# Kernel optimization log

Measured on AMD Instinct MI355X. Metric: run time of the kernel, lower is better.

The kernel has to match this reference:

```python
import jax, jax.numpy as jnp
import numpy as np

B, S, D, H = 4, 1024, 1024, 16
HD = D // H  # head_dim = 64


def setup_inputs() -> dict:
    key = jax.random.key(0)
    ks = jax.random.split(key, 12)
    scale = 1.0 / np.sqrt(D)
    inp = {
        "query": jax.random.normal(ks[0], (B, S, D), jnp.float32),
        "key": jax.random.normal(ks[1], (B, S, D), jnp.float32),
        "value": jax.random.normal(ks[2], (B, S, D), jnp.float32),
        "mask": jnp.zeros((B, S), dtype=bool),  # accepted but unused by the module
        "Wq": jax.random.normal(ks[3], (D, D), jnp.float32) * scale,
        "bq": jnp.zeros((D,), jnp.float32),
        "Wk": jax.random.normal(ks[4], (D, D), jnp.float32) * scale,
        "bk": jnp.zeros((D,), jnp.float32),
        "Wv": jax.random.normal(ks[5], (D, D), jnp.float32) * scale,
        "bv": jnp.zeros((D,), jnp.float32),
        "Wo": jax.random.normal(ks[6], (D, D), jnp.float32) * scale,
        "bo": jnp.zeros((D,), jnp.float32),
    }
    return inp


def _split_heads(x):
    # [B,S,D] -> [B,H,S,HD]
    b, s, _ = x.shape
    return x.reshape(b, s, H, HD).transpose(0, 2, 1, 3)


def reference(query, key, value, mask, Wq, bq, Wk, bk, Wv, bv, Wo, bo):
    b, s, _ = query.shape
    q = _split_heads(query @ Wq.T + bq)
    k = _split_heads(key @ Wk.T + bk)
    v = _split_heads(value @ Wv.T + bv)
    # dense scores, then hollow mask: triu(diag=1) and tril(diag=-1) are both
    # filled with -inf, leaving ONLY the diagonal unmasked
    scores = jnp.einsum("bhqd,bhkd->bhqk", q, k) / jnp.sqrt(jnp.float32(HD))
    diag = jnp.eye(s, dtype=bool)  # the only surviving positions
    scores = jnp.where(diag, scores, -jnp.inf)
    attn = jax.nn.softmax(scores, axis=-1)  # == identity one-hot rows
    out = jnp.einsum("bhqk,bhkd->bhqd", attn, v)
    out = out.transpose(0, 2, 1, 3).reshape(b, s, H * HD)
    return out @ Wo.T + bo
```

## Files before the change

### kernel.cpp

```cpp
#include <hip/hip_runtime.h>
#include <stdint.h>


typedef __attribute__((ext_vector_type(4))) float f32x4;
typedef __attribute__((ext_vector_type(8))) __bf16 bf16x8;
typedef __attribute__((ext_vector_type(4))) float float4v;
typedef __attribute__((ext_vector_type(8))) unsigned short ushort8;
typedef __attribute__((ext_vector_type(4))) unsigned short us4;

#define DEVINL __device__ __forceinline__

DEVINL unsigned short f2bf(float f) {
  union { float f; uint32_t u; } c; c.f = f;
  uint32_t r = c.u + 0x7FFFu + ((c.u >> 16) & 1u);
  return (unsigned short)(r >> 16);
}

#define GLD16(g, l) __builtin_amdgcn_global_load_lds( \
    (__attribute__((address_space(1))) void*)(g),     \
    (__attribute__((address_space(3))) void*)(l), 16, 0, 0)

__global__ __launch_bounds__(256) void prep(
    const float* __restrict__ V, const float* __restrict__ Wv,
    const float* __restrict__ Wo, const float* __restrict__ bv,
    const float* __restrict__ bo,
    unsigned short* __restrict__ Vb, unsigned short* __restrict__ Wob,
    unsigned short* __restrict__ WvT, float* __restrict__ bias2) {
  __shared__ unsigned short tile[64][65];
  const int b = blockIdx.x, t = threadIdx.x;
  if (b < 2560) {
    const float* src = (b < 2048) ? V : Wo;
    unsigned short* dst = (b < 2048) ? Vb : Wob;
    long off = ((long)(b < 2048 ? b : b - 2048) * 256 + t) * 8;
    float4v a = *(const float4v*)(src + off);
    float4v c = *(const float4v*)(src + off + 4);
    ushort8 o;
    o[0]=f2bf(a[0]); o[1]=f2bf(a[1]); o[2]=f2bf(a[2]); o[3]=f2bf(a[3]);
    o[4]=f2bf(c[0]); o[5]=f2bf(c[1]); o[6]=f2bf(c[2]); o[7]=f2bf(c[3]);
    *(ushort8*)(dst + off) = o;
  } else if (b < 2816) {
    const int tb = b - 2560;
    const int c0 = (tb & 15) * 64, j0 = (tb >> 4) * 64;
    const int tr = t >> 4, tc = (t & 15) * 4;
    #pragma unroll
    for (int rr = 0; rr < 4; ++rr) {
      int row = tr + rr * 16;
      float4v v = *(const float4v*)(Wv + (long)(j0 + row) * 1024 + c0 + tc);
      tile[row][tc+0] = f2bf(v[0]);
      tile[row][tc+1] = f2bf(v[1]);
      tile[row][tc+2] = f2bf(v[2]);
      tile[row][tc+3] = f2bf(v[3]);
    }
    __syncthreads();
    #pragma unroll
    for (int rr = 0; rr < 4; ++rr) {
      int crow = tr + rr * 16;
      us4 o;
      #pragma unroll
      for (int i = 0; i < 4; ++i) o[i] = tile[tc + i][crow];
      *(us4*)(WvT + (long)(c0 + crow) * 1024 + j0 + tc) = o;
    }
  } else {
    const int tb = b - 2816;
    const int w = t >> 6, lane = t & 63;
    const int row = tb * 4 + w;
    float s = 0.f;
    #pragma unroll
    for (int c = 0; c < 4; ++c) {
      int col = c * 256 + lane * 4;
      float4v a = *(const float4v*)(Wo + (long)row * 1024 + col);
      float4v x = *(const float4v*)(bv + col);
      s += a[0]*x[0] + a[1]*x[1] + a[2]*x[2] + a[3]*x[3];
    }
    #pragma unroll
    for (int off = 32; off; off >>= 1) s += __shfl_down(s, off);
    if (lane == 0) bias2[row] = s + bo[row];
  }
}

template<int BM, int BN, int NT, int WM, int WN, int OUT_BF16, int ADD_BIAS>
__global__ __launch_bounds__(NT) void gemm_nt(
    const unsigned short* __restrict__ A,
    const unsigned short* __restrict__ B,
    const float* __restrict__ bias,
    void* __restrict__ Cv) {
  constexpr int K = 1024, N = 1024;
  constexpr int NBN = N / BN;
  constexpr int SM = BM / WM, SN = BN / WN;
  constexpr int FM = SM / 16, FN = SN / 16;
  constexpr int CA = BM * 8 / NT, CB = BN * 8 / NT;
  constexpr int NKT = K / 64;

  __shared__ alignas(16) unsigned short lA[2][BM * 64];
  __shared__ alignas(16) unsigned short lB[2][BN * 64];

  const int t = threadIdx.x;
  const int bm = blockIdx.x / NBN;
  const int bn = blockIdx.x % NBN;
  const int m0 = bm * BM, n0 = bn * BN;

  long gAoff[CA]; int lAoff[CA];
  #pragma unroll
  for (int c = 0; c < CA; ++c) {
    int s = c * NT + t, r = s >> 3, sl = (s & 7) ^ (r & 7);
    gAoff[c] = (long)(m0 + r) * K + sl * 8;
    lAoff[c] = s * 8;
  }
  long gBoff[CB]; int lBoff[CB];
  #pragma unroll
  for (int c = 0; c < CB; ++c) {
    int s = c * NT + t, r = s >> 3, sl = (s & 7) ^ (r & 7);
    gBoff[c] = (long)(n0 + r) * K + sl * 8;
    lBoff[c] = s * 8;
  }

  const int lane = t & 63;
  const int w = t >> 6, wm = w / WN, wn = w % WN;
  const int fr = lane & 15, fq = lane >> 4;

  int aoff[FM][2], boff[FN][2];
  #pragma unroll
  for (int m = 0; m < FM; ++m) {
    int row = wm * SM + m * 16 + fr;
    #pragma unroll
    for (int h = 0; h < 2; ++h)
      aoff[m][h] = row * 128 + (((h * 4 + fq) ^ (row & 7)) * 16);
  }
  #pragma unroll
  for (int n = 0; n < FN; ++n) {
    int row = wn * SN + n * 16 + fr;
    #pragma unroll
    for (int h = 0; h < 2; ++h)
      boff[n][h] = row * 128 + (((h * 4 + fq) ^ (row & 7)) * 16);
  }

  f32x4 acc[FM][FN] = {};

  #pragma unroll
  for (int c = 0; c < CA; ++c) GLD16(A + gAoff[c], (unsigned short*)lA[0] + lAoff[c]);
  #pragma unroll
  for (int c = 0; c < CB; ++c) GLD16(B + gBoff[c], (unsigned short*)lB[0] + lBoff[c]);
  __syncthreads();

  int cur = 0;
  #pragma unroll 1
  for (int kt = 0; kt < NKT; ++kt) {
    if (kt + 1 < NKT) {
      #pragma unroll
      for (int c = 0; c < CA; ++c)
        GLD16(A + gAoff[c] + (kt + 1) * 64, (unsigned short*)lA[cur ^ 1] + lAoff[c]);
      #pragma unroll
      for (int c = 0; c < CB; ++c)
        GLD16(B + gBoff[c] + (kt + 1) * 64, (unsigned short*)lB[cur ^ 1] + lBoff[c]);
    }
    const char* lAb = (const char*)lA[cur];
    const char* lBb = (const char*)lB[cur];
    bf16x8 av[FM][2], bw[FN][2];
    #pragma unroll
    for (int m = 0; m < FM; ++m)
      #pragma unroll
      for (int h = 0; h < 2; ++h)
        av[m][h] = *(const bf16x8*)(lAb + aoff[m][h]);
    #pragma unroll
    for (int n = 0; n < FN; ++n)
      #pragma unroll
      for (int h = 0; h < 2; ++h)
        bw[n][h] = *(const bf16x8*)(lBb + boff[n][h]);

    #pragma unroll
    for (int m = 0; m < FM; ++m)
      #pragma unroll
      for (int n = 0; n < FN; ++n)
        #pragma unroll
        for (int h = 0; h < 2; ++h)
          acc[m][n] = __builtin_amdgcn_mfma_f32_16x16x32_bf16(
              av[m][h], bw[n][h], acc[m][n], 0, 0, 0);

    __syncthreads();
    cur ^= 1;
  }

  #pragma unroll
  for (int m = 0; m < FM; ++m) {
    #pragma unroll
    for (int n = 0; n < FN; ++n) {
      int gr = m0 + wm * SM + m * 16 + fq * 4;
      int gc = n0 + wn * SN + n * 16 + fr;
      float bb = 0.f;
      if (ADD_BIAS) bb = bias[gc];
      if (OUT_BF16) {
        unsigned short* C = (unsigned short*)Cv;
        #pragma unroll
        for (int j = 0; j < 4; ++j)
          C[(long)(gr + j) * N + gc] = f2bf(acc[m][n][j] + bb);
      } else {
        float* C = (float*)Cv;
        #pragma unroll
        for (int j = 0; j < 4; ++j)
          C[(long)(gr + j) * N + gc] = acc[m][n][j] + bb;
      }
    }
  }
}

extern "C" void kernel_launch(void* const* d_in, const int* in_sizes, int n_in,
                              void* d_out, int out_size, void* d_ws, size_t ws_size,
                              hipStream_t stream) {
  const float* value = (const float*)d_in[2];
  const float* Wv    = (const float*)d_in[8];
  const float* bv    = (const float*)d_in[9];
  const float* Wo    = (const float*)d_in[10];
  const float* bo    = (const float*)d_in[11];

  char* ws = (char*)d_ws;
  unsigned short* Vb    = (unsigned short*)(ws);
  unsigned short* Wob   = (unsigned short*)(ws + 8388608);
  unsigned short* WvTb  = (unsigned short*)(ws + 10485760);
  unsigned short* Wb    = (unsigned short*)(ws + 12582912);
  float*          bias2 = (float*)(ws + 14680064);
  float* out = (float*)d_out;

  prep<<<3072, 256, 0, stream>>>(value, Wv, Wo, bv, bo, Vb, Wob, WvTb, bias2);
  gemm_nt<64, 64, 512, 2, 4, 1, 0><<<256, 512, 0, stream>>>(Wob, WvTb, nullptr, Wb);
  gemm_nt<128, 64, 512, 4, 2, 0, 1><<<512, 512, 0, stream>>>(Vb, Wb, bias2, out);
}
```

Baseline: 139.0 us.

## Overlap V bf16 conversion with weight GEMM, enlarge main tiles, add XCD remap

Moves the large V fp32-to-bf16 conversion out of the prep kernel and into the same launch as the Wo·Wv weight-fold GEMM, so the conversion blocks run alongside the GEMM's 256 blocks. The main GEMM goes from 128x64 to 128x128 tiles (256 workgroups) with a 2x4 wave layout, and gains an XCD-aware tile remap to improve L2 locality across chiplets. The trade-offs are lower occupancy and possible load imbalance from the larger tiles and the mixed kernel.

```diff
diff --git a/kernel.cpp b/kernel.cpp
--- a/kernel.cpp
+++ b/kernel.cpp
@@ -20,72 +20,14 @@
     (__attribute__((address_space(1))) void*)(g),     \
     (__attribute__((address_space(3))) void*)(l), 16, 0, 0)
 
-__global__ __launch_bounds__(256) void prep(
-    const float* __restrict__ V, const float* __restrict__ Wv,
-    const float* __restrict__ Wo, const float* __restrict__ bv,
-    const float* __restrict__ bo,
-    unsigned short* __restrict__ Vb, unsigned short* __restrict__ Wob,
-    unsigned short* __restrict__ WvT, float* __restrict__ bias2) {
-  __shared__ unsigned short tile[64][65];
-  const int b = blockIdx.x, t = threadIdx.x;
-  if (b < 2560) {
-    const float* src = (b < 2048) ? V : Wo;
-    unsigned short* dst = (b < 2048) ? Vb : Wob;
-    long off = ((long)(b < 2048 ? b : b - 2048) * 256 + t) * 8;
-    float4v a = *(const float4v*)(src + off);
-    float4v c = *(const float4v*)(src + off + 4);
-    ushort8 o;
-    o[0]=f2bf(a[0]); o[1]=f2bf(a[1]); o[2]=f2bf(a[2]); o[3]=f2bf(a[3]);
-    o[4]=f2bf(c[0]); o[5]=f2bf(c[1]); o[6]=f2bf(c[2]); o[7]=f2bf(c[3]);
-    *(ushort8*)(dst + off) = o;
-  } else if (b < 2816) {
-    const int tb = b - 2560;
-    const int c0 = (tb & 15) * 64, j0 = (tb >> 4) * 64;
-    const int tr = t >> 4, tc = (t & 15) * 4;
-    #pragma unroll
-    for (int rr = 0; rr < 4; ++rr) {
-      int row = tr + rr * 16;
-      float4v v = *(const float4v*)(Wv + (long)(j0 + row) * 1024 + c0 + tc);
-      tile[row][tc+0] = f2bf(v[0]);
-      tile[row][tc+1] = f2bf(v[1]);
-      tile[row][tc+2] = f2bf(v[2]);
-      tile[row][tc+3] = f2bf(v[3]);
-    }
-    __syncthreads();
-    #pragma unroll
-    for (int rr = 0; rr < 4; ++rr) {
-      int crow = tr + rr * 16;
-      us4 o;
-      #pragma unroll
-      for (int i = 0; i < 4; ++i) o[i] = tile[tc + i][crow];
-      *(us4*)(WvT + (long)(c0 + crow) * 1024 + j0 + tc) = o;
-    }
-  } else {
-    const int tb = b - 2816;
-    const int w = t >> 6, lane = t & 63;
-    const int row = tb * 4 + w;
-    float s = 0.f;
-    #pragma unroll
-    for (int c = 0; c < 4; ++c) {
-      int col = c * 256 + lane * 4;
-      float4v a = *(const float4v*)(Wo + (long)row * 1024 + col);
-      float4v x = *(const float4v*)(bv + col);
-      s += a[0]*x[0] + a[1]*x[1] + a[2]*x[2] + a[3]*x[3];
-    }
-    #pragma unroll
-    for (int off = 32; off; off >>= 1) s += __shfl_down(s, off);
-    if (lane == 0) bias2[row] = s + bo[row];
-  }
-}
-
-template<int BM, int BN, int NT, int WM, int WN, int OUT_BF16, int ADD_BIAS>
-__global__ __launch_bounds__(NT) void gemm_nt(
-    const unsigned short* __restrict__ A,
-    const unsigned short* __restrict__ B,
-    const float* __restrict__ bias,
-    void* __restrict__ Cv) {
+template<int M, int BM, int BN, int NT, int WM, int WN, int OUT_BF16,
+         int ADD_BIAS, int XCD>
+DEVINL void gemm_body(int bidx, const unsigned short* __restrict__ A,
+                      const unsigned short* __restrict__ B,
+                      const float* __restrict__ bias, void* __restrict__ Cv) {
   constexpr int K = 1024, N = 1024;
   constexpr int NBN = N / BN;
+  constexpr int NWG = (M / BM) * NBN;
   constexpr int SM = BM / WM, SN = BN / WN;
   constexpr int FM = SM / 16, FN = SN / 16;
   constexpr int CA = BM * 8 / NT, CB = BN * 8 / NT;
@@ -95,8 +37,12 @@
   __shared__ alignas(16) unsigned short lB[2][BN * 64];
 
   const int t = threadIdx.x;
-  const int bm = blockIdx.x / NBN;
-  const int bn = blockIdx.x % NBN;
+  int tile = bidx;
+  if (XCD) {
+    tile = (bidx & 7) * (NWG / 8) + (bidx >> 3);
+  }
+  const int bm = tile / NBN;
+  const int bn = tile % NBN;
   const int m0 = bm * BM, n0 = bn * BN;
 
   long gAoff[CA]; int lAoff[CA];
@@ -203,6 +149,86 @@
   }
 }
 
+__global__ __launch_bounds__(256) void prep_small(
+    const float* __restrict__ Wv, const float* __restrict__ Wo,
+    const float* __restrict__ bv, const float* __restrict__ bo,
+    unsigned short* __restrict__ Wob, unsigned short* __restrict__ WvT,
+    float* __restrict__ bias2) {
+  __shared__ unsigned short tile[64][65];
+  const int b = blockIdx.x, t = threadIdx.x;
+  if (b < 512) {
+    long off = ((long)b * 256 + t) * 8;
+    float4v a = *(const float4v*)(Wo + off);
+    float4v c = *(const float4v*)(Wo + off + 4);
+    ushort8 o;
+    o[0]=f2bf(a[0]); o[1]=f2bf(a[1]); o[2]=f2bf(a[2]); o[3]=f2bf(a[3]);
+    o[4]=f2bf(c[0]); o[5]=f2bf(c[1]); o[6]=f2bf(c[2]); o[7]=f2bf(c[3]);
+    *(ushort8*)(Wob + off) = o;
+  } else if (b < 768) {
+    const int tb = b - 512;
+    const int c0 = (tb & 15) * 64, j0 = (tb >> 4) * 64;
+    const int tr = t >> 4, tc = (t & 15) * 4;
+    #pragma unroll
+    for (int rr = 0; rr < 4; ++rr) {
+      int row = tr + rr * 16;
+      float4v v = *(const float4v*)(Wv + (long)(j0 + row) * 1024 + c0 + tc);
+      tile[row][tc+0] = f2bf(v[0]);
+      tile[row][tc+1] = f2bf(v[1]);
+      tile[row][tc+2] = f2bf(v[2]);
+      tile[row][tc+3] = f2bf(v[3]);
+    }
+    __syncthreads();
+    #pragma unroll
+    for (int rr = 0; rr < 4; ++rr) {
+      int crow = tr + rr * 16;
+      us4 o;
+      #pragma unroll
+      for (int i = 0; i < 4; ++i) o[i] = tile[tc + i][crow];
+      *(us4*)(WvT + (long)(c0 + crow) * 1024 + j0 + tc) = o;
+    }
+  } else {
+    const int tb = b - 768;
+    const int w = t >> 6, lane = t & 63;
+    const int row = tb * 4 + w;
+    float s = 0.f;
+    #pragma unroll
+    for (int c = 0; c < 4; ++c) {
+      int col = c * 256 + lane * 4;
+      float4v a = *(const float4v*)(Wo + (long)row * 1024 + col);
+      float4v x = *(const float4v*)(bv + col);
+      s += a[0]*x[0] + a[1]*x[1] + a[2]*x[2] + a[3]*x[3];
+    }
+    #pragma unroll
+    for (int off = 32; off; off >>= 1) s += __shfl_down(s, off);
+    if (lane == 0) bias2[row] = s + bo[row];
+  }
+}
+
+__global__ __launch_bounds__(512) void wgemm_vcvt(
+    const unsigned short* __restrict__ Wob,
+    const unsigned short* __restrict__ WvT,
+    unsigned short* __restrict__ Wb,
+    const float* __restrict__ V, unsigned short* __restrict__ Vb) {
+  const int b = blockIdx.x;
+  if (b < 256) {
+    gemm_body<1024, 64, 64, 512, 2, 4, 1, 0, 0>(b, Wob, WvT, nullptr, Wb);
+  } else {
+    long off = ((long)(b - 256) * 512 + threadIdx.x) * 8;
+    float4v a = *(const float4v*)(V + off);
+    float4v c = *(const float4v*)(V + off + 4);
+    ushort8 o;
+    o[0]=f2bf(a[0]); o[1]=f2bf(a[1]); o[2]=f2bf(a[2]); o[3]=f2bf(a[3]);
+    o[4]=f2bf(c[0]); o[5]=f2bf(c[1]); o[6]=f2bf(c[2]); o[7]=f2bf(c[3]);
+    *(ushort8*)(Vb + off) = o;
+  }
+}
+
+__global__ __launch_bounds__(512) void gemm_main(
+    const unsigned short* __restrict__ A, const unsigned short* __restrict__ B,
+    const float* __restrict__ bias, float* __restrict__ C) {
+  gemm_body<4096, 128, 128, 512, 2, 4, 0, 1, 1>(blockIdx.x, A, B, bias, C);
+}
+
 extern "C" void kernel_launch(void* const* d_in, const int* in_sizes, int n_in,
                               void* d_out, int out_size, void* d_ws, size_t ws_size,
                               hipStream_t stream) {
@@ -220,7 +246,7 @@
   float*          bias2 = (float*)(ws + 14680064);
   float* out = (float*)d_out;
 
-  prep<<<3072, 256, 0, stream>>>(value, Wv, Wo, bv, bo, Vb, Wob, WvTb, bias2);
-  gemm_nt<64, 64, 512, 2, 4, 1, 0><<<256, 512, 0, stream>>>(Wob, WvTb, nullptr, Wb);
-  gemm_nt<128, 64, 512, 4, 2, 0, 1><<<512, 512, 0, stream>>>(Vb, Wb, bias2, out);
-}
+  prep_small<<<1024, 256, 0, stream>>>(Wv, Wo, bv, bo, Wob, WvTb, bias2);
+  wgemm_vcvt<<<1280, 512, 0, stream>>>(Wob, WvTb, Wb, value, Vb);
+  gemm_main<<<256, 512, 0, stream>>>(Vb, Wb, bias2, out);
+}
```

Result: no change. 138.9 us (-0.1%).
